# Performance work log

Measured on AMD Instinct MI355X. Metric: run time of the kernel, lower is better.

## Reference

```python
import jax, jax.numpy as jnp
import numpy as np

N = 50000        # number of nodes (A is [N, N] sparse adjacency)
NNZ = 1600000    # number of edges (avg degree 32)
UNITS = 64       # output feature dim


def setup_inputs() -> dict:
    key = jax.random.key(0)
    k1, k2, k3, k4 = jax.random.split(key, 4)
    rows = jax.random.randint(k1, (NNZ,), 0, N, dtype=jnp.int32)
    cols = jax.random.randint(k2, (NNZ,), 0, N, dtype=jnp.int32)
    values = jax.random.uniform(k3, (NNZ,), dtype=jnp.float32)
    # glorot-like scale for kernel of shape (N, UNITS)
    kernel = jax.random.normal(k4, (N, UNITS), dtype=jnp.float32) * np.float32(1.0 / np.sqrt(N))
    bias = jnp.zeros((UNITS,), dtype=jnp.float32)
    return {"rows": rows, "cols": cols, "values": values, "kernel": kernel, "bias": bias}


def reference(rows, cols, values, kernel, bias):
    # Faithful math of: relu(dense(A) @ kernel + bias), computed as SpMM
    # (zeros of the densified A contribute nothing, so results are identical).
    gathered = values[:, None] * kernel[cols]           # [nnz, units]
    out = jax.ops.segment_sum(gathered, rows, num_segments=N)  # [N, units]
    return jax.nn.relu(out + bias)
```

## Files before the change

### kernel.cpp

```cpp
#include <hip/hip_runtime.h>

#define UNITS 64
#define NNODES 50000
#define NBUCK 512
#define CAP 3584
#define BIN_TPB 512
#define BIN_EPT 8
#define PREP_BLOCKS 782
#define SPMM_TPB 1024
#define CSTRIDE 16

typedef unsigned long long u64;
typedef unsigned int u32;
typedef unsigned short u16;


__device__ __forceinline__ int rowbase_of(u32 b) {
    return (int)((b * 50000u + 511u) >> 9);
}

__device__ __forceinline__ u16 f2bf(u32 b) {
    return (u16)((b + 0x7FFFu + ((b >> 16) & 1u)) >> 16);
}

__global__ __launch_bounds__(BIN_TPB) void gc_bin_prep(const int* __restrict__ rows,
                                                       const int* __restrict__ cols,
                                                       const float* __restrict__ values,
                                                       const float* __restrict__ kf,
                                                       u16* __restrict__ kb,
                                                       int* __restrict__ gcursor,
                                                       u64* __restrict__ edges,
                                                       int nnz, int binBlocks) {
    int t = threadIdx.x;
    if ((int)blockIdx.x >= binBlocks) {
        int base = ((blockIdx.x - binBlocks) * BIN_TPB + t) * 8;
        if (base + 8 <= NNODES * UNITS) {
            float4 fa = ((const float4*)(kf + base))[0];
            float4 fb = ((const float4*)(kf + base))[1];
            ushort4 oa, ob;
            oa.x = f2bf(__float_as_uint(fa.x)); oa.y = f2bf(__float_as_uint(fa.y));
            oa.z = f2bf(__float_as_uint(fa.z)); oa.w = f2bf(__float_as_uint(fa.w));
            ob.x = f2bf(__float_as_uint(fb.x)); ob.y = f2bf(__float_as_uint(fb.y));
            ob.z = f2bf(__float_as_uint(fb.z)); ob.w = f2bf(__float_as_uint(fb.w));
            ((ushort4*)(kb + base))[0] = oa;
            ((ushort4*)(kb + base))[1] = ob;
        }
        return;
    }

    __shared__ u64 stage[BIN_TPB * BIN_EPT];
    __shared__ int hist[NBUCK];
    __shared__ int lstart[NBUCK];
    __shared__ int delta[NBUCK];
    __shared__ int wsum[8];
    hist[t] = 0;
    __syncthreads();

    int blockStart = blockIdx.x * (BIN_TPB * BIN_EPT);
    int cnt = min(BIN_TPB * BIN_EPT, nnz - blockStart);
    int base_idx = blockStart + t * BIN_EPT;

    int rr[BIN_EPT];
    int cc[BIN_EPT];
    float vv[BIN_EPT];
    if (base_idx + BIN_EPT <= nnz) {
        int4 ra = ((const int4*)(rows + base_idx))[0];
        int4 rb = ((const int4*)(rows + base_idx))[1];
        int4 ca = ((const int4*)(cols + base_idx))[0];
        int4 cb = ((const int4*)(cols + base_idx))[1];
        float4 va = ((const float4*)(values + base_idx))[0];
        float4 vb = ((const float4*)(values + base_idx))[1];
        rr[0]=ra.x; rr[1]=ra.y; rr[2]=ra.z; rr[3]=ra.w;
        rr[4]=rb.x; rr[5]=rb.y; rr[6]=rb.z; rr[7]=rb.w;
        cc[0]=ca.x; cc[1]=ca.y; cc[2]=ca.z; cc[3]=ca.w;
        cc[4]=cb.x; cc[5]=cb.y; cc[6]=cb.z; cc[7]=cb.w;
        vv[0]=va.x; vv[1]=va.y; vv[2]=va.z; vv[3]=va.w;
        vv[4]=vb.x; vv[5]=vb.y; vv[6]=vb.z; vv[7]=vb.w;
    } else {
#pragma unroll
        for (int k = 0; k < BIN_EPT; ++k) {
            int idx = base_idx + k;
            rr[k] = (idx < nnz) ? rows[idx] : -1;
            cc[k] = (idx < nnz) ? cols[idx] : 0;
            vv[k] = (idx < nnz) ? values[idx] : 0.0f;
        }
    }

    u64 rec[BIN_EPT];
    int bk[BIN_EPT];
    int rk[BIN_EPT];
#pragma unroll
    for (int k = 0; k < BIN_EPT; ++k) {
        if (rr[k] >= 0) {
            int r = rr[k];
            u32 v = __float_as_uint(vv[k]);
            int b = (int)(((u32)r * 512u) / 50000u);
            int lrow = r - rowbase_of((u32)b);
            rec[k] = ((u64)v << 32) | ((u64)(u32)b << 23) | ((u64)(u32)lrow << 16) | (u64)(u32)cc[k];
            bk[k] = b;
            rk[k] = atomicAdd(&hist[b], 1);
        } else {
            bk[k] = -1;
        }
    }
    __syncthreads();

    {
        int wid = t >> 6, ln = t & 63;
        int val = hist[t];
        for (int off = 1; off < 64; off <<= 1) {
            int x = __shfl_up(val, off, 64);
            if (ln >= off) val += x;
        }
        if (ln == 63) wsum[wid] = val;
        __syncthreads();
        if (t == 0) {
            int s = 0;
            for (int i = 0; i < 8; ++i) { int x = wsum[i]; wsum[i] = s; s += x; }
        }
        __syncthreads();
        int incl = val + wsum[wid];
        int excl = incl - hist[t];
        int h = hist[t];
        int gbase = (h > 0) ? (t * CAP + atomicAdd(&gcursor[t * CSTRIDE], h)) : 0;
        delta[t] = gbase - excl;
        lstart[t] = excl;
    }
    __syncthreads();

#pragma unroll
    for (int k = 0; k < BIN_EPT; ++k) {
        if (bk[k] >= 0) stage[lstart[bk[k]] + rk[k]] = rec[k];
    }
    __syncthreads();

    for (int i = t; i < cnt; i += BIN_TPB) {
        u64 r = stage[i];
        int b = (int)((r >> 23) & 0x1FF);
        int gpos = delta[b] + i;
        if (gpos < (b + 1) * CAP) edges[gpos] = r;
    }
}

__global__ __launch_bounds__(SPMM_TPB, 8) void gc_spmm(const u64* __restrict__ edges,
                                                       const int* __restrict__ gcursor,
                                                       const u16* __restrict__ kb,
                                                       const float* __restrict__ bias,
                                                       float* __restrict__ out) {
    __shared__ u64 stage[CAP];
    __shared__ int rhist[128];
    __shared__ int rstart[129];
    __shared__ int wsum2[2];
    int b = blockIdx.x;
    int t = threadIdx.x;
    int rowlo = rowbase_of((u32)b);
    int nrows = rowbase_of((u32)b + 1u) - rowlo;
    int count = min(gcursor[b * CSTRIDE], CAP);
    const u64* eb = edges + (size_t)b * CAP;

    if (t < 128) rhist[t] = 0;
    __syncthreads();

    u64 rec[4];
    int rk[4], lr[4];
#pragma unroll
    for (int k = 0; k < 4; ++k) {
        int i = k * SPMM_TPB + t;
        if (i < count) {
            u64 r = eb[i];
            rec[k] = r;
            int l = (int)((r >> 16) & 0x7F);
            lr[k] = l;
            rk[k] = atomicAdd(&rhist[l], 1);
        } else {
            lr[k] = -1;
        }
    }
    __syncthreads();

    {
        int wid = t >> 6, ln = t & 63;
        int val = (t < 128) ? rhist[t] : 0;
        if (wid < 2) {
            for (int off = 1; off < 64; off <<= 1) {
                int x = __shfl_up(val, off, 64);
                if (ln >= off) val += x;
            }
            if (ln == 63) wsum2[wid] = val;
        }
        __syncthreads();
        if (t == 0) { int a = wsum2[0]; wsum2[0] = 0; wsum2[1] = a; }
        __syncthreads();
        if (wid < 2) rstart[t] = val + wsum2[wid] - rhist[t];
        if (t == 0) rstart[128] = count;
    }
    __syncthreads();

#pragma unroll
    for (int k = 0; k < 4; ++k) {
        if (lr[k] >= 0) stage[rstart[lr[k]] + rk[k]] = rec[k];
    }
    __syncthreads();

    int uq = t & 15;
    int g  = t >> 4;
    float4 bl = ((const float4*)bias)[uq];
    const u16* kbq = kb + 4 * uq;

    for (int row = g; row < nrows; row += 64) {
        int j0 = rstart[row];
        int e  = rstart[row + 1];
        float ax = 0.f, ay = 0.f, az = 0.f, aw = 0.f;
        int j = j0;
        for (; j + 4 <= e; j += 4) {
            u64 r0 = stage[j + 0];
            u64 r1 = stage[j + 1];
            u64 r2 = stage[j + 2];
            u64 r3 = stage[j + 3];
            u64 q0 = *(const u64*)(kbq + ((u32)r0 & 0xFFFFu) * UNITS);
            u64 q1 = *(const u64*)(kbq + ((u32)r1 & 0xFFFFu) * UNITS);
            u64 q2 = *(const u64*)(kbq + ((u32)r2 & 0xFFFFu) * UNITS);
            u64 q3 = *(const u64*)(kbq + ((u32)r3 & 0xFFFFu) * UNITS);
            float v0 = __uint_as_float((u32)(r0 >> 32));
            float v1 = __uint_as_float((u32)(r1 >> 32));
            float v2 = __uint_as_float((u32)(r2 >> 32));
            float v3 = __uint_as_float((u32)(r3 >> 32));
            u32 lo, hi;
            lo = (u32)q0; hi = (u32)(q0 >> 32);
            ax = fmaf(v0, __uint_as_float(lo << 16), ax);
            ay = fmaf(v0, __uint_as_float(lo & 0xFFFF0000u), ay);
            az = fmaf(v0, __uint_as_float(hi << 16), az);
            aw = fmaf(v0, __uint_as_float(hi & 0xFFFF0000u), aw);
            lo = (u32)q1; hi = (u32)(q1 >> 32);
            ax = fmaf(v1, __uint_as_float(lo << 16), ax);
            ay = fmaf(v1, __uint_as_float(lo & 0xFFFF0000u), ay);
            az = fmaf(v1, __uint_as_float(hi << 16), az);
            aw = fmaf(v1, __uint_as_float(hi & 0xFFFF0000u), aw);
            lo = (u32)q2; hi = (u32)(q2 >> 32);
            ax = fmaf(v2, __uint_as_float(lo << 16), ax);
            ay = fmaf(v2, __uint_as_float(lo & 0xFFFF0000u), ay);
            az = fmaf(v2, __uint_as_float(hi << 16), az);
            aw = fmaf(v2, __uint_as_float(hi & 0xFFFF0000u), aw);
            lo = (u32)q3; hi = (u32)(q3 >> 32);
            ax = fmaf(v3, __uint_as_float(lo << 16), ax);
            ay = fmaf(v3, __uint_as_float(lo & 0xFFFF0000u), ay);
            az = fmaf(v3, __uint_as_float(hi << 16), az);
            aw = fmaf(v3, __uint_as_float(hi & 0xFFFF0000u), aw);
        }
        for (; j < e; ++j) {
            u64 r = stage[j];
            u64 q = *(const u64*)(kbq + ((u32)r & 0xFFFFu) * UNITS);
            float v = __uint_as_float((u32)(r >> 32));
            u32 lo = (u32)q, hi = (u32)(q >> 32);
            ax = fmaf(v, __uint_as_float(lo << 16), ax);
            ay = fmaf(v, __uint_as_float(lo & 0xFFFF0000u), ay);
            az = fmaf(v, __uint_as_float(hi << 16), az);
            aw = fmaf(v, __uint_as_float(hi & 0xFFFF0000u), aw);
        }
        float4 o;
        o.x = fmaxf(ax + bl.x, 0.0f);
        o.y = fmaxf(ay + bl.y, 0.0f);
        o.z = fmaxf(az + bl.z, 0.0f);
        o.w = fmaxf(aw + bl.w, 0.0f);
        ((float4*)out)[(size_t)(rowlo + row) * 16 + uq] = o;
    }
}

extern "C" void kernel_launch(void* const* d_in, const int* in_sizes, int n_in,
                              void* d_out, int out_size, void* d_ws, size_t ws_size,
                              hipStream_t stream) {
    const int*   rows   = (const int*)d_in[0];
    const int*   cols   = (const int*)d_in[1];
    const float* values = (const float*)d_in[2];
    const float* kern   = (const float*)d_in[3];
    const float* bias   = (const float*)d_in[4];
    float* out = (float*)d_out;

    const int nnz = in_sizes[0];

    char* ws = (char*)d_ws;
    u16* kb      = (u16*)(ws + 0);
    int* gcursor = (int*)(ws + 6400000);
    u64* edges   = (u64*)(ws + 6432768);

    hipMemsetAsync(gcursor, 0, NBUCK * CSTRIDE * sizeof(int), stream);

    int binBlocks = (nnz + BIN_TPB * BIN_EPT - 1) / (BIN_TPB * BIN_EPT);
    gc_bin_prep<<<binBlocks + PREP_BLOCKS, BIN_TPB, 0, stream>>>(
        rows, cols, values, kern, kb, gcursor, edges, nnz, binBlocks);

    gc_spmm<<<NBUCK, SPMM_TPB, 0, stream>>>(edges, gcursor, kb, bias, out);
}
```

Baseline: 118.3 us.

## Split each SpMM bucket across two half-size blocks by row parity

The SpMM kernel now launches two 512-thread blocks per bucket, each handling the rows of one parity (even or odd local row). Each block reads every edge in the bucket with 16-byte paired loads but keeps only the edges for its own rows, histograms them into 64 bins, and scatters them into a smaller shared stage. The aim is more, smaller blocks with less shared memory each, for better occupancy and load balance across CUs. The cost is that every edge record is read twice from global memory, plus a re-read during the scatter; edges beyond the reduced stage size are silently dropped.

```diff
diff --git a/kernel.cpp b/kernel.cpp
--- a/kernel.cpp
+++ b/kernel.cpp
@@ -7,7 +7,8 @@
 #define BIN_TPB 512
 #define BIN_EPT 8
 #define PREP_BLOCKS 782
-#define SPMM_TPB 1024
+#define SPMM_TPB 512
+#define STG 1920
 #define CSTRIDE 16
 
 typedef unsigned long long u64;
@@ -147,58 +148,72 @@
                                                        const u16* __restrict__ kb,
                                                        const float* __restrict__ bias,
                                                        float* __restrict__ out) {
-    __shared__ u64 stage[CAP];
-    __shared__ int rhist[128];
-    __shared__ int rstart[129];
-    __shared__ int wsum2[2];
-    int b = blockIdx.x;
-    int t = threadIdx.x;
-    int rowlo = rowbase_of((u32)b);
-    int nrows = rowbase_of((u32)b + 1u) - rowlo;
-    int count = min(gcursor[b * CSTRIDE], CAP);
-    const u64* eb = edges + (size_t)b * CAP;
-
-    if (t < 128) rhist[t] = 0;
-    __syncthreads();
-
-    u64 rec[4];
-    int rk[4], lr[4];
+    __shared__ u64 stage[STG];
+    __shared__ int rhist[64];
+    __shared__ int rstart[65];
+    int blk = blockIdx.x;
+    int bkt = blk >> 1;
+    int h   = blk & 1;
+    int t   = threadIdx.x;
+    int rowlo = rowbase_of((u32)bkt);
+    int nrows = rowbase_of((u32)bkt + 1u) - rowlo;
+    int nrowsh = (nrows - h + 1) >> 1;
+    int count = min(gcursor[bkt * CSTRIDE], CAP);
+    const u64* eb = edges + (size_t)bkt * CAP;
+
+    if (t < 64) rhist[t] = 0;
+    __syncthreads();
+
+    int meta[8];
 #pragma unroll
     for (int k = 0; k < 4; ++k) {
-        int i = k * SPMM_TPB + t;
-        if (i < count) {
-            u64 r = eb[i];
-            rec[k] = r;
-            int l = (int)((r >> 16) & 0x7F);
-            lr[k] = l;
-            rk[k] = atomicAdd(&rhist[l], 1);
-        } else {
-            lr[k] = -1;
-        }
-    }
-    __syncthreads();
-
-    {
-        int wid = t >> 6, ln = t & 63;
-        int val = (t < 128) ? rhist[t] : 0;
-        if (wid < 2) {
-            for (int off = 1; off < 64; off <<= 1) {
-                int x = __shfl_up(val, off, 64);
-                if (ln >= off) val += x;
+        int i = k * 1024 + 2 * t;
+        u64 r0 = 0, r1 = 0;
+        int n = 0;
+        if (i + 2 <= count) {
+            ulonglong2 p = ((const ulonglong2*)(eb + i))[0];
+            r0 = p.x; r1 = p.y; n = 2;
+        } else if (i < count) {
+            r0 = eb[i]; n = 1;
+        }
+        meta[2 * k] = -1; meta[2 * k + 1] = -1;
+        if (n >= 1) {
+            int lrow = (int)((r0 >> 16) & 0x7F);
+            if ((lrow & 1) == h) {
+                int lri = lrow >> 1;
+                meta[2 * k] = (lri << 16) | atomicAdd(&rhist[lri], 1);
             }
-            if (ln == 63) wsum2[wid] = val;
-        }
-        __syncthreads();
-        if (t == 0) { int a = wsum2[0]; wsum2[0] = 0; wsum2[1] = a; }
-        __syncthreads();
-        if (wid < 2) rstart[t] = val + wsum2[wid] - rhist[t];
-        if (t == 0) rstart[128] = count;
-    }
-    __syncthreads();
-
-#pragma unroll
-    for (int k = 0; k < 4; ++k) {
-        if (lr[k] >= 0) stage[rstart[lr[k]] + rk[k]] = rec[k];
+        }
+        if (n == 2) {
+            int lrow = (int)((r1 >> 16) & 0x7F);
+            if ((lrow & 1) == h) {
+                int lri = lrow >> 1;
+                meta[2 * k + 1] = (lri << 16) | atomicAdd(&rhist[lri], 1);
+            }
+        }
+    }
+    __syncthreads();
+
+    if (t < 64) {
+        int val = rhist[t];
+        int incl = val;
+        for (int off = 1; off < 64; off <<= 1) {
+            int x = __shfl_up(incl, off, 64);
+            if (t >= off) incl += x;
+        }
+        rstart[t] = incl - val;
+        if (t == 63) rstart[64] = incl;
+    }
+    __syncthreads();
+
+#pragma unroll
+    for (int k = 0; k < 8; ++k) {
+        int m = meta[k];
+        if (m >= 0) {
+            int i = (k >> 1) * 1024 + 2 * t + (k & 1);
+            int pos = rstart[m >> 16] + (m & 0xFFFF);
+            if (pos < STG) stage[pos] = eb[i];
+        }
     }
     __syncthreads();
 
@@ -207,9 +222,9 @@
     float4 bl = ((const float4*)bias)[uq];
     const u16* kbq = kb + 4 * uq;
 
-    for (int row = g; row < nrows; row += 64) {
-        int j0 = rstart[row];
-        int e  = rstart[row + 1];
+    for (int lri = g; lri < nrowsh; lri += 32) {
+        int j0 = min(rstart[lri], STG);
+        int e  = min(rstart[lri + 1], STG);
         float ax = 0.f, ay = 0.f, az = 0.f, aw = 0.f;
         int j = j0;
         for (; j + 4 <= e; j += 4) {
@@ -262,6 +277,7 @@
         o.y = fmaxf(ay + bl.y, 0.0f);
         o.z = fmaxf(az + bl.z, 0.0f);
         o.w = fmaxf(aw + bl.w, 0.0f);
+        int row = (lri << 1) + h;
         ((float4*)out)[(size_t)(rowlo + row) * 16 + uq] = o;
     }
 }
@@ -289,5 +305,5 @@
     gc_bin_prep<<<binBlocks + PREP_BLOCKS, BIN_TPB, 0, stream>>>(
         rows, cols, values, kern, kb, gcursor, edges, nnz, binBlocks);
 
-    gc_spmm<<<NBUCK, SPMM_TPB, 0, stream>>>(edges, gcursor, kb, bias, out);
-}
+    gc_spmm<<<2 * NBUCK, SPMM_TPB, 0, stream>>>(edges, gcursor, kb, bias, out);
+}
```

New measurement: 122.1 us. 1.03x slower.

## Fuse binning and SpMM into one cooperative kernel with grid sync

Applied to the files above, without the earlier changes.

Merges the bin/prep kernel and the SpMM kernel into a single cooperative launch of 512 blocks of 512 threads. The bf16 kernel conversion becomes a grid-stride loop, and each block bins a contiguous segment of edges. After a grid-wide sync, each block processes its own bucket. This removes a kernel launch boundary and its drain/fill gap. In exchange it halves the threads per SpMM block (1024 to 512), adds grid-sync overhead, and keeps a two-launch fallback if the cooperative launch fails.

```diff
diff --git a/kernel.cpp b/kernel.cpp
--- a/kernel.cpp
+++ b/kernel.cpp
@@ -1,13 +1,14 @@
 #include <hip/hip_runtime.h>
+#include <hip/hip_cooperative_groups.h>
 
 #define UNITS 64
 #define NNODES 50000
 #define NBUCK 512
 #define CAP 3584
-#define BIN_TPB 512
-#define BIN_EPT 8
-#define PREP_BLOCKS 782
-#define SPMM_TPB 1024
+#define TPB 512
+#define GRID 512
+#define EPTA 7
+#define EPTB 7
 #define CSTRIDE 16
 
 typedef unsigned long long u64;
@@ -23,18 +24,28 @@
     return (u16)((b + 0x7FFFu + ((b >> 16) & 1u)) >> 16);
 }
 
-__global__ __launch_bounds__(BIN_TPB) void gc_bin_prep(const int* __restrict__ rows,
-                                                       const int* __restrict__ cols,
-                                                       const float* __restrict__ values,
-                                                       const float* __restrict__ kf,
-                                                       u16* __restrict__ kb,
-                                                       int* __restrict__ gcursor,
-                                                       u64* __restrict__ edges,
-                                                       int nnz, int binBlocks) {
+__global__ __launch_bounds__(TPB, 4) void gc_fused(const int* __restrict__ rows,
+                                                   const int* __restrict__ cols,
+                                                   const float* __restrict__ values,
+                                                   const float* __restrict__ kf,
+                                                   u16* __restrict__ kb,
+                                                   int* __restrict__ gcursor,
+                                                   u64* __restrict__ edges,
+                                                   const float* __restrict__ bias,
+                                                   float* __restrict__ out,
+                                                   int nnz, int mode) {
+    __shared__ u64 stage[CAP];
+    __shared__ int hist[NBUCK];
+    __shared__ int lstart[NBUCK];
+    __shared__ int delta[NBUCK];
+    __shared__ int wsum[8];
+
     int t = threadIdx.x;
-    if ((int)blockIdx.x >= binBlocks) {
-        int base = ((blockIdx.x - binBlocks) * BIN_TPB + t) * 8;
-        if (base + 8 <= NNODES * UNITS) {
+    int bid = blockIdx.x;
+
+    if (mode != 2) {
+        for (int u8 = bid * TPB + t; u8 < (NNODES * UNITS) / 8; u8 += GRID * TPB) {
+            int base = u8 * 8;
             float4 fa = ((const float4*)(kf + base))[0];
             float4 fb = ((const float4*)(kf + base))[1];
             ushort4 oa, ob;
@@ -45,160 +56,122 @@
             ((ushort4*)(kb + base))[0] = oa;
             ((ushort4*)(kb + base))[1] = ob;
         }
-        return;
-    }
-
-    __shared__ u64 stage[BIN_TPB * BIN_EPT];
-    __shared__ int hist[NBUCK];
-    __shared__ int lstart[NBUCK];
-    __shared__ int delta[NBUCK];
-    __shared__ int wsum[8];
-    hist[t] = 0;
-    __syncthreads();
-
-    int blockStart = blockIdx.x * (BIN_TPB * BIN_EPT);
-    int cnt = min(BIN_TPB * BIN_EPT, nnz - blockStart);
-    int base_idx = blockStart + t * BIN_EPT;
-
-    int rr[BIN_EPT];
-    int cc[BIN_EPT];
-    float vv[BIN_EPT];
-    if (base_idx + BIN_EPT <= nnz) {
-        int4 ra = ((const int4*)(rows + base_idx))[0];
-        int4 rb = ((const int4*)(rows + base_idx))[1];
-        int4 ca = ((const int4*)(cols + base_idx))[0];
-        int4 cb = ((const int4*)(cols + base_idx))[1];
-        float4 va = ((const float4*)(values + base_idx))[0];
-        float4 vb = ((const float4*)(values + base_idx))[1];
-        rr[0]=ra.x; rr[1]=ra.y; rr[2]=ra.z; rr[3]=ra.w;
-        rr[4]=rb.x; rr[5]=rb.y; rr[6]=rb.z; rr[7]=rb.w;
-        cc[0]=ca.x; cc[1]=ca.y; cc[2]=ca.z; cc[3]=ca.w;
-        cc[4]=cb.x; cc[5]=cb.y; cc[6]=cb.z; cc[7]=cb.w;
-        vv[0]=va.x; vv[1]=va.y; vv[2]=va.z; vv[3]=va.w;
-        vv[4]=vb.x; vv[5]=vb.y; vv[6]=vb.z; vv[7]=vb.w;
-    } else {
-#pragma unroll
-        for (int k = 0; k < BIN_EPT; ++k) {
-            int idx = base_idx + k;
-            rr[k] = (idx < nnz) ? rows[idx] : -1;
-            cc[k] = (idx < nnz) ? cols[idx] : 0;
-            vv[k] = (idx < nnz) ? values[idx] : 0.0f;
-        }
-    }
-
-    u64 rec[BIN_EPT];
-    int bk[BIN_EPT];
-    int rk[BIN_EPT];
-#pragma unroll
-    for (int k = 0; k < BIN_EPT; ++k) {
-        if (rr[k] >= 0) {
-            int r = rr[k];
-            u32 v = __float_as_uint(vv[k]);
-            int b = (int)(((u32)r * 512u) / 50000u);
-            int lrow = r - rowbase_of((u32)b);
-            rec[k] = ((u64)v << 32) | ((u64)(u32)b << 23) | ((u64)(u32)lrow << 16) | (u64)(u32)cc[k];
-            bk[k] = b;
-            rk[k] = atomicAdd(&hist[b], 1);
-        } else {
+
+        hist[t] = 0;
+        __syncthreads();
+
+        int seg = (nnz + GRID - 1) / GRID;
+        int blockStart = bid * seg;
+        int cnt = min(seg, max(0, nnz - blockStart));
+
+        u64 rec[EPTA];
+        int bk[EPTA];
+        int rk[EPTA];
+#pragma unroll
+        for (int k = 0; k < EPTA; ++k) {
+            int idx = blockStart + k * TPB + t;
             bk[k] = -1;
-        }
-    }
-    __syncthreads();
-
-    {
-        int wid = t >> 6, ln = t & 63;
-        int val = hist[t];
-        for (int off = 1; off < 64; off <<= 1) {
-            int x = __shfl_up(val, off, 64);
-            if (ln >= off) val += x;
-        }
-        if (ln == 63) wsum[wid] = val;
-        __syncthreads();
-        if (t == 0) {
-            int s = 0;
-            for (int i = 0; i < 8; ++i) { int x = wsum[i]; wsum[i] = s; s += x; }
-        }
-        __syncthreads();
-        int incl = val + wsum[wid];
-        int excl = incl - hist[t];
-        int h = hist[t];
-        int gbase = (h > 0) ? (t * CAP + atomicAdd(&gcursor[t * CSTRIDE], h)) : 0;
-        delta[t] = gbase - excl;
-        lstart[t] = excl;
-    }
-    __syncthreads();
-
-#pragma unroll
-    for (int k = 0; k < BIN_EPT; ++k) {
-        if (bk[k] >= 0) stage[lstart[bk[k]] + rk[k]] = rec[k];
-    }
-    __syncthreads();
-
-    for (int i = t; i < cnt; i += BIN_TPB) {
-        u64 r = stage[i];
-        int b = (int)((r >> 23) & 0x1FF);
-        int gpos = delta[b] + i;
-        if (gpos < (b + 1) * CAP) edges[gpos] = r;
-    }
-}
-
-__global__ __launch_bounds__(SPMM_TPB, 8) void gc_spmm(const u64* __restrict__ edges,
-                                                       const int* __restrict__ gcursor,
-                                                       const u16* __restrict__ kb,
-                                                       const float* __restrict__ bias,
-                                                       float* __restrict__ out) {
-    __shared__ u64 stage[CAP];
-    __shared__ int rhist[128];
-    __shared__ int rstart[129];
-    __shared__ int wsum2[2];
-    int b = blockIdx.x;
-    int t = threadIdx.x;
+            if (k * TPB + t < cnt) {
+                int r = rows[idx];
+                int c = cols[idx];
+                u32 v = __float_as_uint(values[idx]);
+                int b = (int)(((u32)r * 512u) / 50000u);
+                int lrow = r - rowbase_of((u32)b);
+                rec[k] = ((u64)v << 32) | ((u64)(u32)b << 23) | ((u64)(u32)lrow << 16) | (u64)(u32)c;
+                bk[k] = b;
+                rk[k] = atomicAdd(&hist[b], 1);
+            }
+        }
+        __syncthreads();
+
+        {
+            int wid = t >> 6, ln = t & 63;
+            int val = hist[t];
+            for (int off = 1; off < 64; off <<= 1) {
+                int x = __shfl_up(val, off, 64);
+                if (ln >= off) val += x;
+            }
+            if (ln == 63) wsum[wid] = val;
+            __syncthreads();
+            if (t == 0) {
+                int s = 0;
+                for (int i = 0; i < 8; ++i) { int x = wsum[i]; wsum[i] = s; s += x; }
+            }
+            __syncthreads();
+            int incl = val + wsum[wid];
+            int excl = incl - hist[t];
+            int h = hist[t];
+            int gbase = (h > 0) ? (t * CAP + atomicAdd(&gcursor[t * CSTRIDE], h)) : 0;
+            delta[t] = gbase - excl;
+            lstart[t] = excl;
+        }
+        __syncthreads();
+
+#pragma unroll
+        for (int k = 0; k < EPTA; ++k) {
+            if (bk[k] >= 0) stage[lstart[bk[k]] + rk[k]] = rec[k];
+        }
+        __syncthreads();
+
+        for (int i = t; i < cnt; i += TPB) {
+            u64 r = stage[i];
+            int b = (int)((r >> 23) & 0x1FF);
+            int gpos = delta[b] + i;
+            if (gpos < (b + 1) * CAP) edges[gpos] = r;
+        }
+
+        if (mode == 1) return;
+        __threadfence();
+        cooperative_groups::this_grid().sync();
+        __syncthreads();
+    }
+
+    int b = bid;
     int rowlo = rowbase_of((u32)b);
     int nrows = rowbase_of((u32)b + 1u) - rowlo;
     int count = min(gcursor[b * CSTRIDE], CAP);
     const u64* eb = edges + (size_t)b * CAP;
 
-    if (t < 128) rhist[t] = 0;
-    __syncthreads();
-
-    u64 rec[4];
-    int rk[4], lr[4];
-#pragma unroll
-    for (int k = 0; k < 4; ++k) {
-        int i = k * SPMM_TPB + t;
+    if (t < 128) hist[t] = 0;
+    __syncthreads();
+
+    u64 recB[EPTB];
+    int rkB[EPTB], lrB[EPTB];
+#pragma unroll
+    for (int k = 0; k < EPTB; ++k) {
+        int i = k * TPB + t;
+        lrB[k] = -1;
         if (i < count) {
             u64 r = eb[i];
-            rec[k] = r;
+            recB[k] = r;
             int l = (int)((r >> 16) & 0x7F);
-            lr[k] = l;
-            rk[k] = atomicAdd(&rhist[l], 1);
-        } else {
-            lr[k] = -1;
+            lrB[k] = l;
+            rkB[k] = atomicAdd(&hist[l], 1);
         }
     }
     __syncthreads();
 
     {
         int wid = t >> 6, ln = t & 63;
-        int val = (t < 128) ? rhist[t] : 0;
+        int val = (t < 128) ? hist[t] : 0;
         if (wid < 2) {
             for (int off = 1; off < 64; off <<= 1) {
                 int x = __shfl_up(val, off, 64);
                 if (ln >= off) val += x;
             }
-            if (ln == 63) wsum2[wid] = val;
-        }
-        __syncthreads();
-        if (t == 0) { int a = wsum2[0]; wsum2[0] = 0; wsum2[1] = a; }
-        __syncthreads();
-        if (wid < 2) rstart[t] = val + wsum2[wid] - rhist[t];
-        if (t == 0) rstart[128] = count;
-    }
-    __syncthreads();
-
-#pragma unroll
-    for (int k = 0; k < 4; ++k) {
-        if (lr[k] >= 0) stage[rstart[lr[k]] + rk[k]] = rec[k];
+            if (ln == 63) wsum[wid] = val;
+        }
+        __syncthreads();
+        if (t == 0) { int a = wsum[0]; wsum[0] = 0; wsum[1] = a; }
+        __syncthreads();
+        if (wid < 2) lstart[t] = val + wsum[wid] - hist[t];
+        if (t == 0) lstart[128] = count;
+    }
+    __syncthreads();
+
+#pragma unroll
+    for (int k = 0; k < EPTB; ++k) {
+        if (lrB[k] >= 0) stage[lstart[lrB[k]] + rkB[k]] = recB[k];
     }
     __syncthreads();
 
@@ -207,9 +180,9 @@
     float4 bl = ((const float4*)bias)[uq];
     const u16* kbq = kb + 4 * uq;
 
-    for (int row = g; row < nrows; row += 64) {
-        int j0 = rstart[row];
-        int e  = rstart[row + 1];
+    for (int row = g; row < nrows; row += 32) {
+        int j0 = lstart[row];
+        int e  = lstart[row + 1];
         float ax = 0.f, ay = 0.f, az = 0.f, aw = 0.f;
         int j = j0;
         for (; j + 4 <= e; j += 4) {
@@ -276,7 +249,7 @@
     const float* bias   = (const float*)d_in[4];
     float* out = (float*)d_out;
 
-    const int nnz = in_sizes[0];
+    int nnz = in_sizes[0];
 
     char* ws = (char*)d_ws;
     u16* kb      = (u16*)(ws + 0);
@@ -285,9 +258,16 @@
 
     hipMemsetAsync(gcursor, 0, NBUCK * CSTRIDE * sizeof(int), stream);
 
-    int binBlocks = (nnz + BIN_TPB * BIN_EPT - 1) / (BIN_TPB * BIN_EPT);
-    gc_bin_prep<<<binBlocks + PREP_BLOCKS, BIN_TPB, 0, stream>>>(
-        rows, cols, values, kern, kb, gcursor, edges, nnz, binBlocks);
-
-    gc_spmm<<<NBUCK, SPMM_TPB, 0, stream>>>(edges, gcursor, kb, bias, out);
-}
+    int mode0 = 0, mode1 = 1, mode2 = 2;
+    void* args0[] = {(void*)&rows, (void*)&cols, (void*)&values, (void*)&kern,
+                     (void*)&kb, (void*)&gcursor, (void*)&edges, (void*)&bias,
+                     (void*)&out, (void*)&nnz, (void*)&mode0};
+    hipError_t err = hipLaunchCooperativeKernel((const void*)gc_fused, dim3(GRID),
+                                                dim3(TPB), args0, 0, stream);
+    if (err != hipSuccess) {
+        gc_fused<<<GRID, TPB, 0, stream>>>(rows, cols, values, kern, kb, gcursor,
+                                           edges, bias, out, nnz, mode1);
+        gc_fused<<<GRID, TPB, 0, stream>>>(rows, cols, values, kern, kb, gcursor,
+                                           edges, bias, out, nnz, mode2);
+    }
+}
```

New measurement: 306.6 us. 2.59x slower.
